# Performance work log

Measured on AMD Instinct MI355X. Metric: run time of the kernel, lower is better.

Reference implementation:

```python
import jax, jax.numpy as jnp
import numpy as np

N_CELL, N_WELL = 200000, 512
E_CC, E_CW = 1600000, 65536
CF, WF, ED, H = 12, 8, 1, 64
NEG_SLOPE = 0.2


def _p(k, shape, fan_in):
    return jax.random.normal(k, shape, jnp.float32) * (1.0 / np.sqrt(fan_in))


def setup_inputs() -> dict:
    key = jax.random.key(0)
    ks = jax.random.split(key, 32)
    d = {}
    d['cell_x'] = jax.random.normal(ks[0], (N_CELL, CF), jnp.float32)
    d['well_x'] = jax.random.normal(ks[1], (N_WELL, WF), jnp.float32)
    d['c2c_edge_attr'] = jax.random.normal(ks[2], (E_CC, ED), jnp.float32)
    d['c2c_edge_index'] = jax.random.randint(ks[3], (2, E_CC), 0, N_CELL)
    cw_src = jax.random.randint(ks[4], (E_CW,), 0, N_CELL)
    cw_dst = jax.random.randint(ks[5], (E_CW,), 0, N_WELL)
    d['c2w_edge_index'] = jnp.stack([cw_src, cw_dst])
    d['W_cell_emb'] = _p(ks[6], (CF, H), CF)
    d['b_cell_emb'] = jnp.zeros((H,), jnp.float32)
    d['W_well_emb'] = _p(ks[7], (WF, H), WF)
    d['b_well_emb'] = jnp.zeros((H,), jnp.float32)
    d['W_edge_emb'] = _p(ks[8], (ED, H), ED)
    d['b_edge_emb'] = jnp.zeros((H,), jnp.float32)
    d['conv_lin'] = _p(ks[9], (3, H, H), H)
    d['conv_lin_edge'] = _p(ks[10], (3, H, H), H)
    d['conv_att_src'] = _p(ks[11], (3, H), H)
    d['conv_att_dst'] = _p(ks[12], (3, H), H)
    d['conv_att_edge'] = _p(ks[13], (3, H), H)
    d['conv_bias'] = jnp.zeros((3, H), jnp.float32)
    d['wc_lin'] = _p(ks[14], (H, H), H)
    d['wc_att_src'] = _p(ks[15], (H,), H)
    d['wc_att_dst'] = _p(ks[16], (H,), H)
    d['wc_bias'] = jnp.zeros((H,), jnp.float32)
    d['mlp_W1'] = _p(ks[17], (H, H), H)
    d['mlp_b1'] = jnp.zeros((H,), jnp.float32)
    d['mlp_W2'] = _p(ks[18], (H, 75), H)
    d['mlp_b2'] = jnp.zeros((75,), jnp.float32)
    return d


def segment_softmax(logits, seg, num_segments):
    m = jax.ops.segment_max(logits, seg, num_segments=num_segments)
    m = jnp.where(jnp.isfinite(m), m, 0.0)  # empty segments -> 0
    e = jnp.exp(logits - m[seg])
    s = jax.ops.segment_sum(e, seg, num_segments=num_segments)
    return e / s[seg]


def gat_layer(h_src, h_dst, src, dst, lin, att_s, att_d, bias, num_dst,
              edge_feat=None, lin_edge=None, att_e=None):
    # PyG GATConv, heads=1, concat=False, add_self_loops=False
    hs = h_src @ lin                      # [Ns, H]
    hd = hs if h_dst is h_src else h_dst @ lin
    alpha = (hs @ att_s)[src] + (hd @ att_d)[dst]  # [E]
    if edge_feat is not None:
        alpha = alpha + (edge_feat @ lin_edge) @ att_e
    alpha = jax.nn.leaky_relu(alpha, NEG_SLOPE)
    p = segment_softmax(alpha, dst, num_dst)       # scatter-softmax per dst
    out = jax.ops.segment_sum(hs[src] * p[:, None], dst, num_segments=num_dst)
    return out + bias


def reference(cell_x, well_x, c2c_edge_attr,
              W_cell_emb, b_cell_emb, W_well_emb, b_well_emb,
              W_edge_emb, b_edge_emb,
              conv_lin, conv_lin_edge, conv_att_src, conv_att_dst,
              conv_att_edge, conv_bias,
              wc_lin, wc_att_src, wc_att_dst, wc_bias,
              mlp_W1, mlp_b1, mlp_W2, mlp_b2,
              c2c_edge_index, c2w_edge_index):
    h_c = cell_x @ W_cell_emb + b_cell_emb
    h_w = well_x @ W_well_emb + b_well_emb
    ea = c2c_edge_attr @ W_edge_emb + b_edge_emb
    src, dst = c2c_edge_index[0], c2c_edge_index[1]
    n_cell = h_c.shape[0]
    for l in range(3):
        h_c = jax.nn.relu(
            gat_layer(h_c, h_c, src, dst, conv_lin[l], conv_att_src[l],
                      conv_att_dst[l], conv_bias[l], n_cell,
                      edge_feat=ea, lin_edge=conv_lin_edge[l],
                      att_e=conv_att_edge[l]))
    ws, wd = c2w_edge_index[0], c2w_edge_index[1]
    h_well = gat_layer(h_c, h_w, ws, wd, wc_lin, wc_att_src, wc_att_dst,
                       wc_bias, h_w.shape[0])
    out = jax.nn.relu(h_well @ mlp_W1 + mlp_b1) @ mlp_W2 + mlp_b2
    return out.reshape(-1, 3, 25)
```

## Files before the change

### kernel.cpp

```cpp
#include <hip/hip_runtime.h>
#include <hip/hip_fp16.h>
#include <math.h>

__device__ __forceinline__ float wsum(float v){
  #pragma unroll
  for (int o=32;o;o>>=1) v += __shfl_xor(v,o);
  return v;
}

__global__ void k_edge_scalars(const float* __restrict__ lin_edge,
                               const float* __restrict__ att_e,
                               const float* __restrict__ Wrow,
                               const float* __restrict__ bemb,
                               float* __restrict__ escal){
  int l = threadIdx.x >> 6, j = threadIdx.x & 63;
  float v = 0.f;
  for (int k=0;k<64;++k) v = fmaf(lin_edge[l*4096 + j*64 + k], att_e[l*64+k], v);
  float sv = wsum(Wrow[j]*v);
  float ov = wsum(bemb[j]*v);
  if (j==0){ escal[l]=sv; escal[3+l]=ov; }
}

__global__ void k_prepA(const float* __restrict__ W_cell, const float* __restrict__ b_cell,
                        const float* __restrict__ lin0, float* __restrict__ weff){
  int t = threadIdx.x;
  for (int o=t; o<832; o+=256){
    float acc = 0.f;
    if (o < 768){
      int r = o >> 6, c2 = o & 63;
      for (int c=0;c<64;++c) acc = fmaf(W_cell[r*64+c], lin0[c*64+c2], acc);
    } else {
      int c2 = o - 768;
      for (int c=0;c<64;++c) acc = fmaf(b_cell[c], lin0[c*64+c2], acc);
    }
    weff[o] = acc;
  }
}

__global__ void k_prepB(const float* __restrict__ W_well, const float* __restrict__ b_well,
                        const float* __restrict__ wc_lin, const float* __restrict__ att_d,
                        float* __restrict__ wprep){
  __shared__ float tmp[64];
  int t = threadIdx.x;
  if (t < 64){
    float a = 0.f;
    for (int c=0;c<64;++c) a = fmaf(wc_lin[t*64+c], att_d[c], a);
    tmp[t] = a;
  }
  __syncthreads();
  if (t < 9){
    float a = 0.f;
    if (t < 8){ for (int k=0;k<64;++k) a = fmaf(W_well[t*64+k], tmp[k], a); }
    else      { for (int k=0;k<64;++k) a = fmaf(b_well[k],     tmp[k], a); }
    wprep[t] = a;
  }
}

__global__ void k_well_ad2(const float* __restrict__ well_x, const float* __restrict__ wprep,
                           float* __restrict__ ad_w, int n){
  int w = blockIdx.x*blockDim.x + threadIdx.x;
  if (w >= n) return;
  float a = wprep[8];
  #pragma unroll
  for (int r=0;r<8;++r) a = fmaf(well_x[w*8+r], wprep[r], a);
  ad_w[w] = a;
}

__global__ void k_count(const int* __restrict__ dst, int* __restrict__ deg,
                        int* __restrict__ off, int e){
  int i = blockIdx.x*blockDim.x + threadIdx.x;
  if (i<e) off[i] = atomicAdd(&deg[dst[i]], 1);
}

__global__ void k_scan1(const int* __restrict__ deg, int* __restrict__ row1,
                        int* __restrict__ part, int n){
  __shared__ int sm[256];
  int i = blockIdx.x*256 + threadIdx.x;
  int v = (i<n) ? deg[i] : 0;
  sm[threadIdx.x] = v; __syncthreads();
  for (int o=1;o<256;o<<=1){
    int t = (threadIdx.x>= (unsigned)o) ? sm[threadIdx.x-o] : 0;
    __syncthreads();
    sm[threadIdx.x] += t; __syncthreads();
  }
  if (i<n) row1[i] = sm[threadIdx.x];
  if (threadIdx.x==255) part[blockIdx.x] = sm[255];
}

__global__ void k_scan2(int* __restrict__ part, int np){
  __shared__ int sm[1024];
  int t = threadIdx.x;
  sm[t] = (t<np) ? part[t] : 0; __syncthreads();
  for (int o=1;o<1024;o<<=1){
    int v = (t>=o) ? sm[t-o] : 0;
    __syncthreads();
    sm[t] += v; __syncthreads();
  }
  if (t<np) part[t] = (t==0) ? 0 : sm[t-1];
}

__global__ void k_scan3(int* __restrict__ rowptr, const int* __restrict__ part, int n){
  int i = blockIdx.x*256 + threadIdx.x;
  if (i<n) rowptr[i+1] += part[blockIdx.x];
  if (i==0) rowptr[0]=0;
}

__global__ void k_scan_single(const int* __restrict__ deg, int* __restrict__ rowptr, int n){
  __shared__ int sm[1024];
  int t = threadIdx.x;
  sm[t] = (t<n) ? deg[t] : 0; __syncthreads();
  for (int o=1;o<blockDim.x;o<<=1){
    int v = (t>=o)?sm[t-o]:0; __syncthreads();
    sm[t]+=v; __syncthreads();
  }
  if (t<n) rowptr[t+1]=sm[t];
  if (t==0) rowptr[0]=0;
}

__global__ void k_fill_cc(const int* __restrict__ src, const int* __restrict__ dst,
                          const float* __restrict__ attr, const int* __restrict__ rowptr,
                          const int* __restrict__ off, int2* __restrict__ slot, int e){
  int i = blockIdx.x*blockDim.x + threadIdx.x;
  if (i>=e) return;
  int d = dst[i];
  int pos = rowptr[d] + off[i];
  slot[pos] = make_int2(src[i], __float_as_int(attr[i]));
}

__global__ void k_fill_w(const int* __restrict__ src, const int* __restrict__ dst,
                         const int* __restrict__ rowptr, const int* __restrict__ off,
                         int* __restrict__ slot, int e){
  int i = blockIdx.x*blockDim.x + threadIdx.x;
  if (i>=e) return;
  int d = dst[i];
  slot[rowptr[d] + off[i]] = src[i];
}

__global__ __launch_bounds__(256) void k_gemm64(
    const float* __restrict__ h, const float* __restrict__ W,
    const float* __restrict__ att_s, const float* __restrict__ att_d,
    __half* __restrict__ hs, float* __restrict__ as_, float* __restrict__ ad_, int n){
  __shared__ float Ws[64*64];
  __shared__ float hT[64][68];
  int t = threadIdx.x;
  int n0 = blockIdx.x * 64;
  #pragma unroll
  for (int i=t;i<4096;i+=256) Ws[i] = W[i];
  for (int i=t;i<1024;i+=256){
    int node = i >> 4, k4 = (i & 15) << 2;
    int gn = n0 + node;
    float4 v = (gn < n) ? *(const float4*)&h[(size_t)gn*64 + k4] : make_float4(0,0,0,0);
    hT[k4+0][node]=v.x; hT[k4+1][node]=v.y; hT[k4+2][node]=v.z; hT[k4+3][node]=v.w;
  }
  __syncthreads();
  int tx = t & 15, ty = t >> 4;
  int f4 = tx*4;
  float acc[4][4] = {};
  for (int k=0;k<64;++k){
    float4 wv = *(const float4*)&Ws[k*64 + f4];
    float4 hv = *(const float4*)&hT[k][ty*4];
    float hvv[4] = {hv.x,hv.y,hv.z,hv.w};
    float wvv[4] = {wv.x,wv.y,wv.z,wv.w};
    #pragma unroll
    for (int i=0;i<4;++i)
      #pragma unroll
      for (int j=0;j<4;++j)
        acc[i][j] = fmaf(hvv[i], wvv[j], acc[i][j]);
  }
  float4 s4 = *(const float4*)&att_s[f4];
  float4 d4 = *(const float4*)&att_d[f4];
  #pragma unroll
  for (int i=0;i<4;++i){
    int gn = n0 + ty*4 + i;
    if (gn < n){
      union { __half2 h2; unsigned u; } lo, hi;
      lo.h2 = __floats2half2_rn(acc[i][0], acc[i][1]);
      hi.h2 = __floats2half2_rn(acc[i][2], acc[i][3]);
      *(int2*)&hs[(size_t)gn*64 + f4] = make_int2((int)lo.u, (int)hi.u);
      float sv = acc[i][0]*s4.x + acc[i][1]*s4.y + acc[i][2]*s4.z + acc[i][3]*s4.w;
      float dv = acc[i][0]*d4.x + acc[i][1]*d4.y + acc[i][2]*d4.z + acc[i][3]*d4.w;
      #pragma unroll
      for (int o=8;o;o>>=1){ sv += __shfl_xor(sv,o); dv += __shfl_xor(dv,o); }
      if (tx==0){ as_[gn]=sv; ad_[gn]=dv; }
    }
  }
}

__global__ __launch_bounds__(256) void k_gemm_l0(
    const float* __restrict__ x, const float* __restrict__ weff,
    const float* __restrict__ att_s, const float* __restrict__ att_d,
    __half* __restrict__ hs, float* __restrict__ as_, float* __restrict__ ad_, int n){
  __shared__ float Ws[12*64];
  __shared__ float xT[12][68];
  int t = threadIdx.x;
  int n0 = blockIdx.x * 64;
  for (int i=t;i<768;i+=256){
    Ws[i] = weff[i];
    int node = i / 12, r = i - node*12;
    int gn = n0 + node;
    xT[r][node] = (gn < n) ? x[(size_t)gn*12 + r] : 0.f;
  }
  __syncthreads();
  int tx = t & 15, ty = t >> 4;
  int f4 = tx*4;
  float4 be = *(const float4*)&weff[768 + f4];
  float acc[4][4];
  #pragma unroll
  for (int i=0;i<4;++i){ acc[i][0]=be.x; acc[i][1]=be.y; acc[i][2]=be.z; acc[i][3]=be.w; }
  #pragma unroll
  for (int k=0;k<12;++k){
    float4 wv = *(const float4*)&Ws[k*64 + f4];
    float hvv[4];
    #pragma unroll
    for (int i=0;i<4;++i) hvv[i] = xT[k][ty*4+i];
    float wvv[4] = {wv.x,wv.y,wv.z,wv.w};
    #pragma unroll
    for (int i=0;i<4;++i)
      #pragma unroll
      for (int j=0;j<4;++j)
        acc[i][j] = fmaf(hvv[i], wvv[j], acc[i][j]);
  }
  float4 s4 = *(const float4*)&att_s[f4];
  float4 d4 = *(const float4*)&att_d[f4];
  #pragma unroll
  for (int i=0;i<4;++i){
    int gn = n0 + ty*4 + i;
    if (gn < n){
      union { __half2 h2; unsigned u; } lo, hi;
      lo.h2 = __floats2half2_rn(acc[i][0], acc[i][1]);
      hi.h2 = __floats2half2_rn(acc[i][2], acc[i][3]);
      *(int2*)&hs[(size_t)gn*64 + f4] = make_int2((int)lo.u, (int)hi.u);
      float sv = acc[i][0]*s4.x + acc[i][1]*s4.y + acc[i][2]*s4.z + acc[i][3]*s4.w;
      float dv = acc[i][0]*d4.x + acc[i][1]*d4.y + acc[i][2]*d4.z + acc[i][3]*d4.w;
      #pragma unroll
      for (int o=8;o;o>>=1){ sv += __shfl_xor(sv,o); dv += __shfl_xor(dv,o); }
      if (tx==0){ as_[gn]=sv; ad_[gn]=dv; }
    }
  }
}

template<int NA, bool ATTR, bool RELU>
__global__ __launch_bounds__(256) void k_gat_agg2(
    const int* __restrict__ rowptr, const void* __restrict__ slots_v,
    float* __restrict__ alpha_ws,
    const float* __restrict__ as_, const float* __restrict__ ad_,
    const __half* __restrict__ hs, const float* __restrict__ bias,
    const float* __restrict__ escal, int l,
    float* __restrict__ out, int n){
  const int2* slot2 = (const int2*)slots_v;
  const int*  slot1 = (const int*)slots_v;
  int t = threadIdx.x;
  int g = t & 15;
  int node = blockIdx.x*16 + (t >> 4);
  if (node >= n) return;
  int beg = rowptr[node], end = rowptr[node+1];
  float4 b4 = *(const float4*)&bias[g*4];
  if (end == beg){
    float4 r = b4;
    if (RELU){ r.x=fmaxf(r.x,0.f); r.y=fmaxf(r.y,0.f); r.z=fmaxf(r.z,0.f); r.w=fmaxf(r.w,0.f); }
    *(float4*)&out[(size_t)node*64 + g*4] = r;
    return;
  }
  float se = 0.f, oe = 0.f;
  if (ATTR){ se = escal[l]; oe = escal[3+l]; }
  float adn = ad_[node];
  float areg[NA]; int sreg[NA];
  float m = -1e30f;
  #pragma unroll
  for (int it=0; it<NA; ++it){
    int k = beg + it*16 + g;
    areg[it] = -1e30f; sreg[it] = 0;
    if (k < end){
      int s; float a;
      if (ATTR){
        int2 sv = slot2[k];
        s = sv.x;
        a = as_[s] + adn;
        a = fmaf(__int_as_float(sv.y), se, a) + oe;
      } else {
        s = slot1[k];
        a = as_[s] + adn;
      }
      a = (a >= 0.f) ? a : 0.2f*a;
      areg[it] = a; sreg[it] = s;
      m = fmaxf(m, a);
    }
  }
  for (int k = beg + NA*16 + g; k < end; k += 16){
    int s; float a;
    if (ATTR){
      int2 sv = slot2[k];
      s = sv.x;
      a = as_[s] + adn;
      a = fmaf(__int_as_float(sv.y), se, a) + oe;
    } else {
      s = slot1[k];
      a = as_[s] + adn;
    }
    a = (a >= 0.f) ? a : 0.2f*a;
    alpha_ws[k] = a;
    m = fmaxf(m, a);
  }
  #pragma unroll
  for (int o=8;o;o>>=1) m = fmaxf(m, __shfl_xor(m, o, 16));

  float sum = 0.f;
  float4 acc = make_float4(0.f,0.f,0.f,0.f);
  #pragma unroll
  for (int it=0; it<NA; ++it){
    int base = beg + it*16;
    if (base < end){
      float p = (base + g < end) ? __expf(areg[it] - m) : 0.f;
      sum += p;
      int cnt = min(16, end - base);
      for (int j=0;j<cnt;++j){
        float pj = __shfl(p, j, 16);
        int   sj = __shfl(sreg[it], j, 16);
        int2 hb = *(const int2*)&hs[(size_t)sj*64 + g*4];
        union { unsigned u; __half2 h2; } a0, a1; a0.u = (unsigned)hb.x; a1.u = (unsigned)hb.y;
        float2 f0 = __half22float2(a0.h2);
        float2 f1 = __half22float2(a1.h2);
        acc.x = fmaf(f0.x, pj, acc.x);
        acc.y = fmaf(f0.y, pj, acc.y);
        acc.z = fmaf(f1.x, pj, acc.z);
        acc.w = fmaf(f1.y, pj, acc.w);
      }
    }
  }
  for (int base = beg + NA*16; base < end; base += 16){
    int k = base + g;
    float p = 0.f; int s = 0;
    if (k < end){
      s = ATTR ? slot2[k].x : slot1[k];
      p = __expf(alpha_ws[k] - m);
    }
    sum += p;
    int cnt = min(16, end - base);
    for (int j=0;j<cnt;++j){
      float pj = __shfl(p, j, 16);
      int   sj = __shfl(s, j, 16);
      int2 hb = *(const int2*)&hs[(size_t)sj*64 + g*4];
      union { unsigned u; __half2 h2; } a0, a1; a0.u = (unsigned)hb.x; a1.u = (unsigned)hb.y;
      float2 f0 = __half22float2(a0.h2);
      float2 f1 = __half22float2(a1.h2);
      acc.x = fmaf(f0.x, pj, acc.x);
      acc.y = fmaf(f0.y, pj, acc.y);
      acc.z = fmaf(f1.x, pj, acc.z);
      acc.w = fmaf(f1.y, pj, acc.w);
    }
  }
  #pragma unroll
  for (int o=8;o;o>>=1) sum += __shfl_xor(sum, o, 16);
  float4 r;
  r.x = acc.x/sum + b4.x;
  r.y = acc.y/sum + b4.y;
  r.z = acc.z/sum + b4.z;
  r.w = acc.w/sum + b4.w;
  if (RELU){ r.x=fmaxf(r.x,0.f); r.y=fmaxf(r.y,0.f); r.z=fmaxf(r.z,0.f); r.w=fmaxf(r.w,0.f); }
  *(float4*)&out[(size_t)node*64 + g*4] = r;
}

__global__ __launch_bounds__(128) void k_mlp(const float* __restrict__ h_well,
    const float* __restrict__ W1, const float* __restrict__ b1,
    const float* __restrict__ W2, const float* __restrict__ b2,
    float* __restrict__ out, int n){
  __shared__ float hr[64]; __shared__ float h1[64];
  int w = blockIdx.x, t = threadIdx.x;
  if (t<64) hr[t] = h_well[w*64+t];
  __syncthreads();
  if (t<64){
    float a = b1[t];
    for (int k=0;k<64;++k) a = fmaf(hr[k], W1[k*64+t], a);
    h1[t] = fmaxf(a, 0.f);
  }
  __syncthreads();
  if (t<75){
    float a = b2[t];
    for (int k=0;k<64;++k) a = fmaf(h1[k], W2[k*75+t], a);
    out[w*75+t] = a;
  }
}

extern "C" void kernel_launch(void* const* d_in, const int* in_sizes, int n_in,
                              void* d_out, int out_size, void* d_ws, size_t ws_size,
                              hipStream_t stream){
  const float* cell_x = (const float*)d_in[0];
  const float* well_x = (const float*)d_in[1];
  const float* eattr  = (const float*)d_in[2];
  const int*   cc_idx = (const int*)d_in[3];
  const int*   cw_idx = (const int*)d_in[4];
  const float* W_cell = (const float*)d_in[5];
  const float* b_cell = (const float*)d_in[6];
  const float* W_well = (const float*)d_in[7];
  const float* b_well = (const float*)d_in[8];
  const float* W_edge = (const float*)d_in[9];
  const float* b_edge = (const float*)d_in[10];
  const float* conv_lin = (const float*)d_in[11];
  const float* conv_lin_edge = (const float*)d_in[12];
  const float* att_src = (const float*)d_in[13];
  const float* att_dst = (const float*)d_in[14];
  const float* att_edge = (const float*)d_in[15];
  const float* conv_bias = (const float*)d_in[16];
  const float* wc_lin = (const float*)d_in[17];
  const float* wc_att_src = (const float*)d_in[18];
  const float* wc_att_dst = (const float*)d_in[19];
  const float* wc_bias = (const float*)d_in[20];
  const float* mlp_W1 = (const float*)d_in[21];
  const float* mlp_b1 = (const float*)d_in[22];
  const float* mlp_W2 = (const float*)d_in[23];
  const float* mlp_b2 = (const float*)d_in[24];

  int n_cell = in_sizes[0]/12;
  int n_well = in_sizes[1]/8;
  int e_cc = in_sizes[2];
  int e_cw = in_sizes[4]/2;

  const int* cc_src = cc_idx;
  const int* cc_dst = cc_idx + e_cc;
  const int* cw_src = cw_idx;
  const int* cw_dst = cw_idx + e_cw;

  char* p = (char*)d_ws;
  auto alloc = [&](size_t bytes)->void*{
    void* r = (void*)p;
    p += (bytes + 255) & ~(size_t)255;
    return r;
  };
  float* h_cur = (float*)alloc((size_t)n_cell*64*4);
  __half* hs   = (__half*)alloc((size_t)n_cell*64*2);
  float* as_   = (float*)alloc((size_t)n_cell*4);
  float* ad_   = (float*)alloc((size_t)n_cell*4);
  int* deg     = (int*)alloc((size_t)n_cell*4);
  int* rowptr  = (int*)alloc((size_t)(n_cell+1)*4);
  int* part    = (int*)alloc(1024*4);
  int* eoff    = (int*)alloc((size_t)e_cc*4);
  int2* slot2  = (int2*)alloc((size_t)e_cc*8);
  float* alpha_ws  = (float*)alloc((size_t)e_cc*4);
  float* ad_w  = (float*)alloc((size_t)n_well*4);
  int* wdeg    = (int*)alloc((size_t)n_well*4);
  int* wrowptr = (int*)alloc((size_t)(n_well+1)*4);
  int* woff    = (int*)alloc((size_t)e_cw*4);
  int* wslot   = (int*)alloc((size_t)e_cw*4);
  float* walpha= (float*)alloc((size_t)e_cw*4);
  float* h_well= (float*)alloc((size_t)n_well*64*4);
  float* escal = (float*)alloc(64);
  float* weff  = (float*)alloc(832*4);
  float* wprep = (float*)alloc(16*4);

  hipMemsetAsync(deg, 0, (size_t)n_cell*4, stream);
  hipMemsetAsync(wdeg, 0, (size_t)n_well*4, stream);

  k_edge_scalars<<<1, 192, 0, stream>>>(conv_lin_edge, att_edge, W_edge, b_edge, escal);
  k_prepA<<<1, 256, 0, stream>>>(W_cell, b_cell, conv_lin, weff);
  k_prepB<<<1, 128, 0, stream>>>(W_well, b_well, wc_lin, wc_att_dst, wprep);

  k_count<<<(e_cc+255)/256, 256, 0, stream>>>(cc_dst, deg, eoff, e_cc);
  int nb = (n_cell+255)/256;
  k_scan1<<<nb, 256, 0, stream>>>(deg, rowptr+1, part, n_cell);
  k_scan2<<<1, 1024, 0, stream>>>(part, nb);
  k_scan3<<<nb, 256, 0, stream>>>(rowptr, part, n_cell);
  k_fill_cc<<<(e_cc+255)/256, 256, 0, stream>>>(cc_src, cc_dst, eattr, rowptr, eoff, slot2, e_cc);

  k_count<<<(e_cw+255)/256, 256, 0, stream>>>(cw_dst, wdeg, woff, e_cw);
  k_scan_single<<<1, 512, 0, stream>>>(wdeg, wrowptr, n_well);
  k_fill_w<<<(e_cw+255)/256, 256, 0, stream>>>(cw_src, cw_dst, wrowptr, woff, wslot, e_cw);

  k_gemm_l0<<<(n_cell+63)/64, 256, 0, stream>>>(cell_x, weff,
      att_src, att_dst, hs, as_, ad_, n_cell);
  k_gat_agg2<4,true,true><<<(n_cell+15)/16, 256, 0, stream>>>(rowptr, slot2,
      alpha_ws, as_, ad_, hs, conv_bias, escal, 0, h_cur, n_cell);

  for (int l=1;l<3;++l){
    k_gemm64<<<(n_cell+63)/64, 256, 0, stream>>>(h_cur, conv_lin + l*4096,
        att_src + l*64, att_dst + l*64, hs, as_, ad_, n_cell);
    k_gat_agg2<4,true,true><<<(n_cell+15)/16, 256, 0, stream>>>(rowptr, slot2,
        alpha_ws, as_, ad_, hs, conv_bias + l*64, escal, l, h_cur, n_cell);
  }

  k_gemm64<<<(n_cell+63)/64, 256, 0, stream>>>(h_cur, wc_lin, wc_att_src, wc_att_dst,
      hs, as_, ad_, n_cell);
  k_well_ad2<<<(n_well+255)/256, 256, 0, stream>>>(well_x, wprep, ad_w, n_well);
  k_gat_agg2<16,false,false><<<(n_well+15)/16, 256, 0, stream>>>(wrowptr, wslot,
      walpha, as_, ad_w, hs, wc_bias, nullptr, 0, h_well, n_well);

  k_mlp<<<n_well, 128, 0, stream>>>(h_well, mlp_W1, mlp_b1, mlp_W2, mlp_b2, (float*)d_out, n_well);
}
```

Baseline: 604.4 us.

## Fuse layer-0 GEMM with degree counting, split atomic counters, merge fill kernels

Layer-0 embedding GEMM, cell-edge degree counting and well-edge degree counting now run in one launch with block ranges assigned to each role. Cell-edge degree atomics are spread over four sub-counters per destination (by edge index mod 4) to reduce atomic contention. The scan builds per-sub-bucket bases, and the two CSR fill kernels are merged into one. This removes several launches and atomic hot spots, at the cost of a 4x larger degree array and an extra flatbase buffer. Edge order within each row changes, which is harmless for softmax aggregation apart from float summation order.

```diff
diff --git a/kernel.cpp b/kernel.cpp
--- a/kernel.cpp
+++ b/kernel.cpp
@@ -66,100 +66,51 @@
   ad_w[w] = a;
 }
 
-__global__ void k_count(const int* __restrict__ dst, int* __restrict__ deg,
-                        int* __restrict__ off, int e){
-  int i = blockIdx.x*blockDim.x + threadIdx.x;
-  if (i<e) off[i] = atomicAdd(&deg[dst[i]], 1);
-}
-
-__global__ void k_scan1(const int* __restrict__ deg, int* __restrict__ row1,
-                        int* __restrict__ part, int n){
-  __shared__ int sm[256];
-  int i = blockIdx.x*256 + threadIdx.x;
-  int v = (i<n) ? deg[i] : 0;
-  sm[threadIdx.x] = v; __syncthreads();
-  for (int o=1;o<256;o<<=1){
-    int t = (threadIdx.x>= (unsigned)o) ? sm[threadIdx.x-o] : 0;
-    __syncthreads();
-    sm[threadIdx.x] += t; __syncthreads();
-  }
-  if (i<n) row1[i] = sm[threadIdx.x];
-  if (threadIdx.x==255) part[blockIdx.x] = sm[255];
-}
-
-__global__ void k_scan2(int* __restrict__ part, int np){
-  __shared__ int sm[1024];
-  int t = threadIdx.x;
-  sm[t] = (t<np) ? part[t] : 0; __syncthreads();
-  for (int o=1;o<1024;o<<=1){
-    int v = (t>=o) ? sm[t-o] : 0;
-    __syncthreads();
-    sm[t] += v; __syncthreads();
-  }
-  if (t<np) part[t] = (t==0) ? 0 : sm[t-1];
-}
-
-__global__ void k_scan3(int* __restrict__ rowptr, const int* __restrict__ part, int n){
-  int i = blockIdx.x*256 + threadIdx.x;
-  if (i<n) rowptr[i+1] += part[blockIdx.x];
-  if (i==0) rowptr[0]=0;
-}
-
-__global__ void k_scan_single(const int* __restrict__ deg, int* __restrict__ rowptr, int n){
-  __shared__ int sm[1024];
-  int t = threadIdx.x;
-  sm[t] = (t<n) ? deg[t] : 0; __syncthreads();
-  for (int o=1;o<blockDim.x;o<<=1){
-    int v = (t>=o)?sm[t-o]:0; __syncthreads();
-    sm[t]+=v; __syncthreads();
-  }
-  if (t<n) rowptr[t+1]=sm[t];
-  if (t==0) rowptr[0]=0;
-}
-
-__global__ void k_fill_cc(const int* __restrict__ src, const int* __restrict__ dst,
-                          const float* __restrict__ attr, const int* __restrict__ rowptr,
-                          const int* __restrict__ off, int2* __restrict__ slot, int e){
-  int i = blockIdx.x*blockDim.x + threadIdx.x;
-  if (i>=e) return;
-  int d = dst[i];
-  int pos = rowptr[d] + off[i];
-  slot[pos] = make_int2(src[i], __float_as_int(attr[i]));
-}
-
-__global__ void k_fill_w(const int* __restrict__ src, const int* __restrict__ dst,
-                         const int* __restrict__ rowptr, const int* __restrict__ off,
-                         int* __restrict__ slot, int e){
-  int i = blockIdx.x*blockDim.x + threadIdx.x;
-  if (i>=e) return;
-  int d = dst[i];
-  slot[rowptr[d] + off[i]] = src[i];
-}
-
-__global__ __launch_bounds__(256) void k_gemm64(
-    const float* __restrict__ h, const float* __restrict__ W,
+__global__ __launch_bounds__(256) void k_mega0(
+    const float* __restrict__ x, const float* __restrict__ weff,
     const float* __restrict__ att_s, const float* __restrict__ att_d,
-    __half* __restrict__ hs, float* __restrict__ as_, float* __restrict__ ad_, int n){
-  __shared__ float Ws[64*64];
-  __shared__ float hT[64][68];
-  int t = threadIdx.x;
-  int n0 = blockIdx.x * 64;
-  #pragma unroll
-  for (int i=t;i<4096;i+=256) Ws[i] = W[i];
-  for (int i=t;i<1024;i+=256){
-    int node = i >> 4, k4 = (i & 15) << 2;
+    __half* __restrict__ hs, float* __restrict__ as_, float* __restrict__ ad_, int n,
+    const int* __restrict__ cc_dst, int* __restrict__ deg4, int* __restrict__ eoff, int e_cc,
+    const int* __restrict__ cw_dst, int* __restrict__ wdeg, int* __restrict__ woff, int e_cw,
+    int gGemm, int gCnt){
+  int b = blockIdx.x;
+  int t = threadIdx.x;
+  if (b >= gGemm){
+    if (b < gGemm + gCnt){
+      int cb = b - gGemm;
+      int stride = gCnt * 256;
+      for (int i = cb*256 + t; i < e_cc; i += stride){
+        int d = cc_dst[i];
+        eoff[i] = atomicAdd(&deg4[(d<<2) | (i&3)], 1);
+      }
+    } else {
+      int i = (b - gGemm - gCnt)*256 + t;
+      if (i < e_cw) woff[i] = atomicAdd(&wdeg[cw_dst[i]], 1);
+    }
+    return;
+  }
+  __shared__ float Ws[12*64];
+  __shared__ float xT[12][68];
+  int n0 = b * 64;
+  for (int i=t;i<768;i+=256){
+    Ws[i] = weff[i];
+    int node = i / 12, r = i - node*12;
     int gn = n0 + node;
-    float4 v = (gn < n) ? *(const float4*)&h[(size_t)gn*64 + k4] : make_float4(0,0,0,0);
-    hT[k4+0][node]=v.x; hT[k4+1][node]=v.y; hT[k4+2][node]=v.z; hT[k4+3][node]=v.w;
+    xT[r][node] = (gn < n) ? x[(size_t)gn*12 + r] : 0.f;
   }
   __syncthreads();
   int tx = t & 15, ty = t >> 4;
   int f4 = tx*4;
-  float acc[4][4] = {};
-  for (int k=0;k<64;++k){
+  float4 be = *(const float4*)&weff[768 + f4];
+  float acc[4][4];
+  #pragma unroll
+  for (int i=0;i<4;++i){ acc[i][0]=be.x; acc[i][1]=be.y; acc[i][2]=be.z; acc[i][3]=be.w; }
+  #pragma unroll
+  for (int k=0;k<12;++k){
     float4 wv = *(const float4*)&Ws[k*64 + f4];
-    float4 hv = *(const float4*)&hT[k][ty*4];
-    float hvv[4] = {hv.x,hv.y,hv.z,hv.w};
+    float hvv[4];
+    #pragma unroll
+    for (int i=0;i<4;++i) hvv[i] = xT[k][ty*4+i];
     float wvv[4] = {wv.x,wv.y,wv.z,wv.w};
     #pragma unroll
     for (int i=0;i<4;++i)
@@ -186,33 +137,108 @@
   }
 }
 
-__global__ __launch_bounds__(256) void k_gemm_l0(
-    const float* __restrict__ x, const float* __restrict__ weff,
+__global__ void k_scan1b(const int* __restrict__ deg4, int* __restrict__ flatbase,
+                         int* __restrict__ part, int n){
+  __shared__ int sm[256];
+  int d = blockIdx.x*256 + threadIdx.x;
+  int4 v = make_int4(0,0,0,0);
+  if (d < n) v = *(const int4*)&deg4[(size_t)d*4];
+  int tot = v.x+v.y+v.z+v.w;
+  sm[threadIdx.x] = tot; __syncthreads();
+  for (int o=1;o<256;o<<=1){
+    int tv = (threadIdx.x >= (unsigned)o) ? sm[threadIdx.x-o] : 0;
+    __syncthreads();
+    sm[threadIdx.x] += tv; __syncthreads();
+  }
+  if (d < n){
+    int base = sm[threadIdx.x] - tot;
+    int4 fb;
+    fb.x = base; fb.y = base + v.x; fb.z = fb.y + v.y; fb.w = fb.z + v.z;
+    *(int4*)&flatbase[(size_t)d*4] = fb;
+  }
+  if (threadIdx.x==255) part[blockIdx.x] = sm[255];
+}
+
+__global__ void k_scan2(int* __restrict__ part, int np){
+  __shared__ int sm[1024];
+  int t = threadIdx.x;
+  sm[t] = (t<np) ? part[t] : 0; __syncthreads();
+  for (int o=1;o<1024;o<<=1){
+    int v = (t>=o) ? sm[t-o] : 0;
+    __syncthreads();
+    sm[t] += v; __syncthreads();
+  }
+  if (t<np) part[t] = (t==0) ? 0 : sm[t-1];
+}
+
+__global__ void k_scan3b(int* __restrict__ flatbase, int* __restrict__ rowptr,
+                         const int* __restrict__ part, int n, int etot){
+  int d = blockIdx.x*256 + threadIdx.x;
+  if (d < n){
+    int pb = part[blockIdx.x];
+    int4 fb = *(int4*)&flatbase[(size_t)d*4];
+    fb.x += pb; fb.y += pb; fb.z += pb; fb.w += pb;
+    *(int4*)&flatbase[(size_t)d*4] = fb;
+    rowptr[d] = fb.x;
+    if (d==0) rowptr[n] = etot;
+  }
+}
+
+__global__ void k_scan_single(const int* __restrict__ deg, int* __restrict__ rowptr, int n){
+  __shared__ int sm[1024];
+  int t = threadIdx.x;
+  sm[t] = (t<n) ? deg[t] : 0; __syncthreads();
+  for (int o=1;o<blockDim.x;o<<=1){
+    int v = (t>=o)?sm[t-o]:0; __syncthreads();
+    sm[t]+=v; __syncthreads();
+  }
+  if (t<n) rowptr[t+1]=sm[t];
+  if (t==0) rowptr[0]=0;
+}
+
+__global__ void k_fill2(const int* __restrict__ cc_src, const int* __restrict__ cc_dst,
+                        const float* __restrict__ attr, const int* __restrict__ flatbase,
+                        const int* __restrict__ eoff, int2* __restrict__ slot, int e_cc,
+                        const int* __restrict__ cw_src, const int* __restrict__ cw_dst,
+                        const int* __restrict__ wrowptr, const int* __restrict__ woff,
+                        int* __restrict__ wslot, int e_cw){
+  int i = blockIdx.x*blockDim.x + threadIdx.x;
+  if (i < e_cc){
+    int d = cc_dst[i];
+    int pos = flatbase[(d<<2) | (i&3)] + eoff[i];
+    slot[pos] = make_int2(cc_src[i], __float_as_int(attr[i]));
+  } else {
+    int j = i - e_cc;
+    if (j < e_cw){
+      wslot[wrowptr[cw_dst[j]] + woff[j]] = cw_src[j];
+    }
+  }
+}
+
+__global__ __launch_bounds__(256) void k_gemm64(
+    const float* __restrict__ h, const float* __restrict__ W,
     const float* __restrict__ att_s, const float* __restrict__ att_d,
     __half* __restrict__ hs, float* __restrict__ as_, float* __restrict__ ad_, int n){
-  __shared__ float Ws[12*64];
-  __shared__ float xT[12][68];
+  __shared__ float Ws[64*64];
+  __shared__ float hT[64][68];
   int t = threadIdx.x;
   int n0 = blockIdx.x * 64;
-  for (int i=t;i<768;i+=256){
-    Ws[i] = weff[i];
-    int node = i / 12, r = i - node*12;
+  #pragma unroll
+  for (int i=t;i<4096;i+=256) Ws[i] = W[i];
+  for (int i=t;i<1024;i+=256){
+    int node = i >> 4, k4 = (i & 15) << 2;
     int gn = n0 + node;
-    xT[r][node] = (gn < n) ? x[(size_t)gn*12 + r] : 0.f;
+    float4 v = (gn < n) ? *(const float4*)&h[(size_t)gn*64 + k4] : make_float4(0,0,0,0);
+    hT[k4+0][node]=v.x; hT[k4+1][node]=v.y; hT[k4+2][node]=v.z; hT[k4+3][node]=v.w;
   }
   __syncthreads();
   int tx = t & 15, ty = t >> 4;
   int f4 = tx*4;
-  float4 be = *(const float4*)&weff[768 + f4];
-  float acc[4][4];
-  #pragma unroll
-  for (int i=0;i<4;++i){ acc[i][0]=be.x; acc[i][1]=be.y; acc[i][2]=be.z; acc[i][3]=be.w; }
-  #pragma unroll
-  for (int k=0;k<12;++k){
+  float acc[4][4] = {};
+  for (int k=0;k<64;++k){
     float4 wv = *(const float4*)&Ws[k*64 + f4];
-    float hvv[4];
-    #pragma unroll
-    for (int i=0;i<4;++i) hvv[i] = xT[k][ty*4+i];
+    float4 hv = *(const float4*)&hT[k][ty*4];
+    float hvv[4] = {hv.x,hv.y,hv.z,hv.w};
     float wvv[4] = {wv.x,wv.y,wv.z,wv.w};
     #pragma unroll
     for (int i=0;i<4;++i)
@@ -430,7 +456,8 @@
   __half* hs   = (__half*)alloc((size_t)n_cell*64*2);
   float* as_   = (float*)alloc((size_t)n_cell*4);
   float* ad_   = (float*)alloc((size_t)n_cell*4);
-  int* deg     = (int*)alloc((size_t)n_cell*4);
+  int* deg4    = (int*)alloc((size_t)n_cell*16);
+  int* flatbase= (int*)alloc((size_t)n_cell*16);
   int* rowptr  = (int*)alloc((size_t)(n_cell+1)*4);
   int* part    = (int*)alloc(1024*4);
   int* eoff    = (int*)alloc((size_t)e_cc*4);
@@ -447,26 +474,29 @@
   float* weff  = (float*)alloc(832*4);
   float* wprep = (float*)alloc(16*4);
 
-  hipMemsetAsync(deg, 0, (size_t)n_cell*4, stream);
+  hipMemsetAsync(deg4, 0, (size_t)n_cell*16, stream);
   hipMemsetAsync(wdeg, 0, (size_t)n_well*4, stream);
 
   k_edge_scalars<<<1, 192, 0, stream>>>(conv_lin_edge, att_edge, W_edge, b_edge, escal);
   k_prepA<<<1, 256, 0, stream>>>(W_cell, b_cell, conv_lin, weff);
   k_prepB<<<1, 128, 0, stream>>>(W_well, b_well, wc_lin, wc_att_dst, wprep);
 
-  k_count<<<(e_cc+255)/256, 256, 0, stream>>>(cc_dst, deg, eoff, e_cc);
+  int gGemm = (n_cell+63)/64;
+  int gCnt  = (e_cc + 1023)/1024;
+  int gCntW = (e_cw + 255)/256;
+  k_mega0<<<gGemm+gCnt+gCntW, 256, 0, stream>>>(cell_x, weff, att_src, att_dst,
+      hs, as_, ad_, n_cell,
+      cc_dst, deg4, eoff, e_cc, cw_dst, wdeg, woff, e_cw, gGemm, gCnt);
+
   int nb = (n_cell+255)/256;
-  k_scan1<<<nb, 256, 0, stream>>>(deg, rowptr+1, part, n_cell);
+  k_scan1b<<<nb, 256, 0, stream>>>(deg4, flatbase, part, n_cell);
   k_scan2<<<1, 1024, 0, stream>>>(part, nb);
-  k_scan3<<<nb, 256, 0, stream>>>(rowptr, part, n_cell);
-  k_fill_cc<<<(e_cc+255)/256, 256, 0, stream>>>(cc_src, cc_dst, eattr, rowptr, eoff, slot2, e_cc);
-
-  k_count<<<(e_cw+255)/256, 256, 0, stream>>>(cw_dst, wdeg, woff, e_cw);
+  k_scan3b<<<nb, 256, 0, stream>>>(flatbase, rowptr, part, n_cell, e_cc);
   k_scan_single<<<1, 512, 0, stream>>>(wdeg, wrowptr, n_well);
-  k_fill_w<<<(e_cw+255)/256, 256, 0, stream>>>(cw_src, cw_dst, wrowptr, woff, wslot, e_cw);
-
-  k_gemm_l0<<<(n_cell+63)/64, 256, 0, stream>>>(cell_x, weff,
-      att_src, att_dst, hs, as_, ad_, n_cell);
+
+  k_fill2<<<(e_cc+e_cw+255)/256, 256, 0, stream>>>(cc_src, cc_dst, eattr, flatbase,
+      eoff, slot2, e_cc, cw_src, cw_dst, wrowptr, woff, wslot, e_cw);
+
   k_gat_agg2<4,true,true><<<(n_cell+15)/16, 256, 0, stream>>>(rowptr, slot2,
       alpha_ws, as_, ad_, hs, conv_bias, escal, 0, h_cur, n_cell);
 
```

After: 636.1 us. 5.2% more time.

## Replace CSR build with fixed-capacity per-node edge slots plus overflow list

Applied to the files above, without the earlier changes.

Cell-to-cell adjacency is now stored in 32 fixed slots per destination node, filled directly with one atomic per edge. The overflow beyond 32 goes to a small global list that the aggregation kernel scans linearly. This removes the count, three-pass scan and fill kernels and the offset buffer, and aggregation now reads the degree array instead of rowptr. In exchange the slot buffer is padded to 32 entries per node, and edges beyond the 8192-entry overflow cap would be silently dropped.

```diff
diff --git a/kernel.cpp b/kernel.cpp
--- a/kernel.cpp
+++ b/kernel.cpp
@@ -1,6 +1,9 @@
 #include <hip/hip_runtime.h>
 #include <hip/hip_fp16.h>
 #include <math.h>
+
+#define CCAP 32
+#define OVF_CAP 8192
 
 __device__ __forceinline__ float wsum(float v){
   #pragma unroll
@@ -66,43 +69,27 @@
   ad_w[w] = a;
 }
 
-__global__ void k_count(const int* __restrict__ dst, int* __restrict__ deg,
-                        int* __restrict__ off, int e){
+__global__ void k_build_cc(const int* __restrict__ src, const int* __restrict__ dst,
+                           const float* __restrict__ attr, int* __restrict__ deg,
+                           int2* __restrict__ slot, int4* __restrict__ ovf,
+                           int* __restrict__ n_ovf, int e){
+  int stride = gridDim.x*blockDim.x;
+  for (int i = blockIdx.x*blockDim.x + threadIdx.x; i < e; i += stride){
+    int d = dst[i];
+    int off = atomicAdd(&deg[d], 1);
+    if (off < CCAP){
+      slot[(d<<5) + off] = make_int2(src[i], __float_as_int(attr[i]));
+    } else {
+      int x = atomicAdd(n_ovf, 1);
+      if (x < OVF_CAP) ovf[x] = make_int4(d, src[i], __float_as_int(attr[i]), 0);
+    }
+  }
+}
+
+__global__ void k_count_w(const int* __restrict__ dst, int* __restrict__ deg,
+                          int* __restrict__ off, int e){
   int i = blockIdx.x*blockDim.x + threadIdx.x;
   if (i<e) off[i] = atomicAdd(&deg[dst[i]], 1);
-}
-
-__global__ void k_scan1(const int* __restrict__ deg, int* __restrict__ row1,
-                        int* __restrict__ part, int n){
-  __shared__ int sm[256];
-  int i = blockIdx.x*256 + threadIdx.x;
-  int v = (i<n) ? deg[i] : 0;
-  sm[threadIdx.x] = v; __syncthreads();
-  for (int o=1;o<256;o<<=1){
-    int t = (threadIdx.x>= (unsigned)o) ? sm[threadIdx.x-o] : 0;
-    __syncthreads();
-    sm[threadIdx.x] += t; __syncthreads();
-  }
-  if (i<n) row1[i] = sm[threadIdx.x];
-  if (threadIdx.x==255) part[blockIdx.x] = sm[255];
-}
-
-__global__ void k_scan2(int* __restrict__ part, int np){
-  __shared__ int sm[1024];
-  int t = threadIdx.x;
-  sm[t] = (t<np) ? part[t] : 0; __syncthreads();
-  for (int o=1;o<1024;o<<=1){
-    int v = (t>=o) ? sm[t-o] : 0;
-    __syncthreads();
-    sm[t] += v; __syncthreads();
-  }
-  if (t<np) part[t] = (t==0) ? 0 : sm[t-1];
-}
-
-__global__ void k_scan3(int* __restrict__ rowptr, const int* __restrict__ part, int n){
-  int i = blockIdx.x*256 + threadIdx.x;
-  if (i<n) rowptr[i+1] += part[blockIdx.x];
-  if (i==0) rowptr[0]=0;
 }
 
 __global__ void k_scan_single(const int* __restrict__ deg, int* __restrict__ rowptr, int n){
@@ -115,16 +102,6 @@
   }
   if (t<n) rowptr[t+1]=sm[t];
   if (t==0) rowptr[0]=0;
-}
-
-__global__ void k_fill_cc(const int* __restrict__ src, const int* __restrict__ dst,
-                          const float* __restrict__ attr, const int* __restrict__ rowptr,
-                          const int* __restrict__ off, int2* __restrict__ slot, int e){
-  int i = blockIdx.x*blockDim.x + threadIdx.x;
-  if (i>=e) return;
-  int d = dst[i];
-  int pos = rowptr[d] + off[i];
-  slot[pos] = make_int2(src[i], __float_as_int(attr[i]));
 }
 
 __global__ void k_fill_w(const int* __restrict__ src, const int* __restrict__ dst,
@@ -239,16 +216,118 @@
   }
 }
 
-template<int NA, bool ATTR, bool RELU>
-__global__ __launch_bounds__(256) void k_gat_agg2(
-    const int* __restrict__ rowptr, const void* __restrict__ slots_v,
-    float* __restrict__ alpha_ws,
+template<bool RELU>
+__global__ __launch_bounds__(256) void k_gat_agg3(
+    const int* __restrict__ deg, const int2* __restrict__ slot,
+    const int4* __restrict__ ovf, const int* __restrict__ n_ovf_p,
     const float* __restrict__ as_, const float* __restrict__ ad_,
     const __half* __restrict__ hs, const float* __restrict__ bias,
     const float* __restrict__ escal, int l,
     float* __restrict__ out, int n){
-  const int2* slot2 = (const int2*)slots_v;
-  const int*  slot1 = (const int*)slots_v;
+  int t = threadIdx.x;
+  int g = t & 15;
+  int node = blockIdx.x*16 + (t >> 4);
+  if (node >= n) return;
+  int degn = deg[node];
+  float4 b4 = *(const float4*)&bias[g*4];
+  if (degn == 0){
+    float4 r = b4;
+    if (RELU){ r.x=fmaxf(r.x,0.f); r.y=fmaxf(r.y,0.f); r.z=fmaxf(r.z,0.f); r.w=fmaxf(r.w,0.f); }
+    *(float4*)&out[(size_t)node*64 + g*4] = r;
+    return;
+  }
+  float se = escal[l], oe = escal[3+l];
+  float adn = ad_[node];
+  int cin = min(degn, CCAP);
+  int sb = node << 5;
+  float areg[2]; int sreg[2];
+  float m = -1e30f;
+  #pragma unroll
+  for (int it=0; it<2; ++it){
+    int k = it*16 + g;
+    areg[it] = -1e30f; sreg[it] = 0;
+    if (k < cin){
+      int2 sv = slot[sb + k];
+      float a = as_[sv.x] + adn;
+      a = fmaf(__int_as_float(sv.y), se, a) + oe;
+      a = (a >= 0.f) ? a : 0.2f*a;
+      areg[it] = a; sreg[it] = sv.x;
+      m = fmaxf(m, a);
+    }
+  }
+  int no = 0;
+  if (degn > CCAP) no = min(*n_ovf_p, OVF_CAP);
+  for (int j=0;j<no;++j){
+    int4 e = ovf[j];
+    if (e.x == node){
+      float a = as_[e.y] + adn;
+      a = fmaf(__int_as_float(e.z), se, a) + oe;
+      a = (a >= 0.f) ? a : 0.2f*a;
+      m = fmaxf(m, a);
+    }
+  }
+  #pragma unroll
+  for (int o=8;o;o>>=1) m = fmaxf(m, __shfl_xor(m, o, 16));
+
+  float sum = 0.f;
+  float4 acc = make_float4(0.f,0.f,0.f,0.f);
+  #pragma unroll
+  for (int it=0; it<2; ++it){
+    int base = it*16;
+    if (base < cin){
+      float p = (base + g < cin) ? __expf(areg[it] - m) : 0.f;
+      sum += p;
+      int cnt = min(16, cin - base);
+      for (int j=0;j<cnt;++j){
+        float pj = __shfl(p, j, 16);
+        int   sj = __shfl(sreg[it], j, 16);
+        int2 hb = *(const int2*)&hs[(size_t)sj*64 + g*4];
+        union { unsigned u; __half2 h2; } a0, a1; a0.u = (unsigned)hb.x; a1.u = (unsigned)hb.y;
+        float2 f0 = __half22float2(a0.h2);
+        float2 f1 = __half22float2(a1.h2);
+        acc.x = fmaf(f0.x, pj, acc.x);
+        acc.y = fmaf(f0.y, pj, acc.y);
+        acc.z = fmaf(f1.x, pj, acc.z);
+        acc.w = fmaf(f1.y, pj, acc.w);
+      }
+    }
+  }
+  for (int j=0;j<no;++j){
+    int4 e = ovf[j];
+    if (e.x == node){
+      float a = as_[e.y] + adn;
+      a = fmaf(__int_as_float(e.z), se, a) + oe;
+      a = (a >= 0.f) ? a : 0.2f*a;
+      float p = __expf(a - m);
+      if (g == 0) sum += p;
+      int2 hb = *(const int2*)&hs[(size_t)e.y*64 + g*4];
+      union { unsigned u; __half2 h2; } a0, a1; a0.u = (unsigned)hb.x; a1.u = (unsigned)hb.y;
+      float2 f0 = __half22float2(a0.h2);
+      float2 f1 = __half22float2(a1.h2);
+      acc.x = fmaf(f0.x, p, acc.x);
+      acc.y = fmaf(f0.y, p, acc.y);
+      acc.z = fmaf(f1.x, p, acc.z);
+      acc.w = fmaf(f1.y, p, acc.w);
+    }
+  }
+  #pragma unroll
+  for (int o=8;o;o>>=1) sum += __shfl_xor(sum, o, 16);
+  float4 r;
+  r.x = acc.x/sum + b4.x;
+  r.y = acc.y/sum + b4.y;
+  r.z = acc.z/sum + b4.z;
+  r.w = acc.w/sum + b4.w;
+  if (RELU){ r.x=fmaxf(r.x,0.f); r.y=fmaxf(r.y,0.f); r.z=fmaxf(r.z,0.f); r.w=fmaxf(r.w,0.f); }
+  *(float4*)&out[(size_t)node*64 + g*4] = r;
+}
+
+template<int NA>
+__global__ __launch_bounds__(256) void k_gat_aggw(
+    const int* __restrict__ rowptr, const int* __restrict__ slot1,
+    float* __restrict__ alpha_ws,
+    const float* __restrict__ as_, const float* __restrict__ ad_,
+    const __half* __restrict__ hs, const float* __restrict__ bias,
+    float* __restrict__ out, int n){
   int t = threadIdx.x;
   int g = t & 15;
   int node = blockIdx.x*16 + (t >> 4);
@@ -256,13 +335,9 @@
   int beg = rowptr[node], end = rowptr[node+1];
   float4 b4 = *(const float4*)&bias[g*4];
   if (end == beg){
-    float4 r = b4;
-    if (RELU){ r.x=fmaxf(r.x,0.f); r.y=fmaxf(r.y,0.f); r.z=fmaxf(r.z,0.f); r.w=fmaxf(r.w,0.f); }
-    *(float4*)&out[(size_t)node*64 + g*4] = r;
+    *(float4*)&out[(size_t)node*64 + g*4] = b4;
     return;
   }
-  float se = 0.f, oe = 0.f;
-  if (ATTR){ se = escal[l]; oe = escal[3+l]; }
   float adn = ad_[node];
   float areg[NA]; int sreg[NA];
   float m = -1e30f;
@@ -271,32 +346,16 @@
     int k = beg + it*16 + g;
     areg[it] = -1e30f; sreg[it] = 0;
     if (k < end){
-      int s; float a;
-      if (ATTR){
-        int2 sv = slot2[k];
-        s = sv.x;
-        a = as_[s] + adn;
-        a = fmaf(__int_as_float(sv.y), se, a) + oe;
-      } else {
-        s = slot1[k];
-        a = as_[s] + adn;
-      }
+      int s = slot1[k];
+      float a = as_[s] + adn;
       a = (a >= 0.f) ? a : 0.2f*a;
       areg[it] = a; sreg[it] = s;
       m = fmaxf(m, a);
     }
   }
   for (int k = beg + NA*16 + g; k < end; k += 16){
-    int s; float a;
-    if (ATTR){
-      int2 sv = slot2[k];
-      s = sv.x;
-      a = as_[s] + adn;
-      a = fmaf(__int_as_float(sv.y), se, a) + oe;
-    } else {
-      s = slot1[k];
-      a = as_[s] + adn;
-    }
+    int s = slot1[k];
+    float a = as_[s] + adn;
     a = (a >= 0.f) ? a : 0.2f*a;
     alpha_ws[k] = a;
     m = fmaxf(m, a);
@@ -330,10 +389,7 @@
   for (int base = beg + NA*16; base < end; base += 16){
     int k = base + g;
     float p = 0.f; int s = 0;
-    if (k < end){
-      s = ATTR ? slot2[k].x : slot1[k];
-      p = __expf(alpha_ws[k] - m);
-    }
+    if (k < end){ s = slot1[k]; p = __expf(alpha_ws[k] - m); }
     sum += p;
     int cnt = min(16, end - base);
     for (int j=0;j<cnt;++j){
@@ -356,7 +412,6 @@
   r.y = acc.y/sum + b4.y;
   r.z = acc.z/sum + b4.z;
   r.w = acc.w/sum + b4.w;
-  if (RELU){ r.x=fmaxf(r.x,0.f); r.y=fmaxf(r.y,0.f); r.z=fmaxf(r.z,0.f); r.w=fmaxf(r.w,0.f); }
   *(float4*)&out[(size_t)node*64 + g*4] = r;
 }
 
@@ -431,11 +486,9 @@
   float* as_   = (float*)alloc((size_t)n_cell*4);
   float* ad_   = (float*)alloc((size_t)n_cell*4);
   int* deg     = (int*)alloc((size_t)n_cell*4);
-  int* rowptr  = (int*)alloc((size_t)(n_cell+1)*4);
-  int* part    = (int*)alloc(1024*4);
-  int* eoff    = (int*)alloc((size_t)e_cc*4);
-  int2* slot2  = (int2*)alloc((size_t)e_cc*8);
-  float* alpha_ws  = (float*)alloc((size_t)e_cc*4);
+  int2* slot2  = (int2*)alloc((size_t)n_cell*CCAP*8);
+  int4* ovf    = (int4*)alloc((size_t)OVF_CAP*16);
+  int* n_ovf   = (int*)alloc(256);
   float* ad_w  = (float*)alloc((size_t)n_well*4);
   int* wdeg    = (int*)alloc((size_t)n_well*4);
   int* wrowptr = (int*)alloc((size_t)(n_well+1)*4);
@@ -449,39 +502,36 @@
 
   hipMemsetAsync(deg, 0, (size_t)n_cell*4, stream);
   hipMemsetAsync(wdeg, 0, (size_t)n_well*4, stream);
+  hipMemsetAsync(n_ovf, 0, 4, stream);
 
   k_edge_scalars<<<1, 192, 0, stream>>>(conv_lin_edge, att_edge, W_edge, b_edge, escal);
   k_prepA<<<1, 256, 0, stream>>>(W_cell, b_cell, conv_lin, weff);
   k_prepB<<<1, 128, 0, stream>>>(W_well, b_well, wc_lin, wc_att_dst, wprep);
 
-  k_count<<<(e_cc+255)/256, 256, 0, stream>>>(cc_dst, deg, eoff, e_cc);
-  int nb = (n_cell+255)/256;
-  k_scan1<<<nb, 256, 0, stream>>>(deg, rowptr+1, part, n_cell);
-  k_scan2<<<1, 1024, 0, stream>>>(part, nb);
-  k_scan3<<<nb, 256, 0, stream>>>(rowptr, part, n_cell);
-  k_fill_cc<<<(e_cc+255)/256, 256, 0, stream>>>(cc_src, cc_dst, eattr, rowptr, eoff, slot2, e_cc);
-
-  k_count<<<(e_cw+255)/256, 256, 0, stream>>>(cw_dst, wdeg, woff, e_cw);
+  int gB = (e_cc + 255)/256; if (gB > 2048) gB = 2048;
+  k_build_cc<<<gB, 256, 0, stream>>>(cc_src, cc_dst, eattr, deg, slot2, ovf, n_ovf, e_cc);
+
+  k_count_w<<<(e_cw+255)/256, 256, 0, stream>>>(cw_dst, wdeg, woff, e_cw);
   k_scan_single<<<1, 512, 0, stream>>>(wdeg, wrowptr, n_well);
   k_fill_w<<<(e_cw+255)/256, 256, 0, stream>>>(cw_src, cw_dst, wrowptr, woff, wslot, e_cw);
 
   k_gemm_l0<<<(n_cell+63)/64, 256, 0, stream>>>(cell_x, weff,
       att_src, att_dst, hs, as_, ad_, n_cell);
-  k_gat_agg2<4,true,true><<<(n_cell+15)/16, 256, 0, stream>>>(rowptr, slot2,
-      alpha_ws, as_, ad_, hs, conv_bias, escal, 0, h_cur, n_cell);
+  k_gat_agg3<true><<<(n_cell+15)/16, 256, 0, stream>>>(deg, slot2, ovf, n_ovf,
+      as_, ad_, hs, conv_bias, escal, 0, h_cur, n_cell);
 
   for (int l=1;l<3;++l){
     k_gemm64<<<(n_cell+63)/64, 256, 0, stream>>>(h_cur, conv_lin + l*4096,
         att_src + l*64, att_dst + l*64, hs, as_, ad_, n_cell);
-    k_gat_agg2<4,true,true><<<(n_cell+15)/16, 256, 0, stream>>>(rowptr, slot2,
-        alpha_ws, as_, ad_, hs, conv_bias + l*64, escal, l, h_cur, n_cell);
+    k_gat_agg3<true><<<(n_cell+15)/16, 256, 0, stream>>>(deg, slot2, ovf, n_ovf,
+        as_, ad_, hs, conv_bias + l*64, escal, l, h_cur, n_cell);
   }
 
   k_gemm64<<<(n_cell+63)/64, 256, 0, stream>>>(h_cur, wc_lin, wc_att_src, wc_att_dst,
       hs, as_, ad_, n_cell);
   k_well_ad2<<<(n_well+255)/256, 256, 0, stream>>>(well_x, wprep, ad_w, n_well);
-  k_gat_agg2<16,false,false><<<(n_well+15)/16, 256, 0, stream>>>(wrowptr, wslot,
-      walpha, as_, ad_w, hs, wc_bias, nullptr, 0, h_well, n_well);
+  k_gat_aggw<16><<<(n_well+15)/16, 256, 0, stream>>>(wrowptr, wslot,
+      walpha, as_, ad_w, hs, wc_bias, h_well, n_well);
 
   k_mlp<<<n_well, 128, 0, stream>>>(h_well, mlp_W1, mlp_b1, mlp_W2, mlp_b2, (float*)d_out, n_well);
 }
```

Result: slower. 616.6 us (+2.0%).
